# Performance work log

Measured on AMD Instinct MI355X. Metric: run time of the kernel, lower is better.

Reference implementation:

```python
import jax, jax.numpy as jnp
import numpy as np

DROPOUT_P = 0.1
SCALE = 0.0625  # 1/sqrt(256)


def setup_inputs() -> dict:
    key = jax.random.key(0)
    kq, kk, kv, km, ku = jax.random.split(key, 5)
    B, Sq, Sk, D, Dv = 64, 1024, 1024, 256, 256
    q = jax.random.normal(kq, (B, Sq, D), dtype=jnp.float32)
    k = jax.random.normal(kk, (B, Sk, D), dtype=jnp.float32)
    v = jax.random.normal(kv, (B, Sk, Dv), dtype=jnp.float32)
    mask = jax.random.randint(km, (B, Sk), 0, 2, dtype=jnp.int32)
    drop_u = jax.random.uniform(ku, (B, Sq, Sk), dtype=jnp.float32)
    return {"q": q, "k": k, "v": v, "mask": mask, "drop_u": drop_u}


def reference(q, k, v, mask, drop_u):
    # attn scores: [B, Sq, Sk]
    attn = jnp.einsum("bqd,bkd->bqk", q, k) * SCALE
    # additive padding mask broadcast over queries
    mmask = -1e9 * (1.0 - mask.astype(attn.dtype))  # [B, Sk]
    attn = attn + mmask[:, None, :]
    attn = jax.nn.softmax(attn, axis=-1)
    # inverted dropout with pre-sampled uniforms (deterministic)
    keep = (drop_u >= DROPOUT_P).astype(attn.dtype) / (1.0 - DROPOUT_P)
    attn = attn * keep
    out = jnp.einsum("bqk,bkv->bqv", attn, v)
    return out
```

## Files before the change

kernel.cpp:

```cpp
#include <hip/hip_runtime.h>
#include <hip/hip_bf16.h>
#include <stdint.h>

typedef __bf16 bf16_t;
typedef bf16_t bf16x8 __attribute__((ext_vector_type(8)));
typedef bf16_t bf16x4 __attribute__((ext_vector_type(4)));
typedef float floatx4 __attribute__((ext_vector_type(4)));

#define B_  64
#define SQ  1024
#define SK  1024
#define D_  256
#define DV  256
#define TK  32
#define NT  32
#define SCALE_F 0.0625f
#define NMASK   (-1.0e9f)
#define KEEP_F  (1.0f/0.9f)
#define THRESH  0.1f

#define AS1(p) ((const __attribute__((address_space(1))) uint32_t*)(p))
#define AS3(p) ((__attribute__((address_space(3))) uint32_t*)(p))

#define RAW_BARRIER() __asm__ volatile("s_barrier" ::: "memory")
#define WAIT_VM(N)    __asm__ volatile("s_waitcnt vmcnt(" #N ")" ::: "memory")
#define WAIT_LGKM0()  __asm__ volatile("s_waitcnt lgkmcnt(0)" ::: "memory")

__device__ __forceinline__ void gload16(const void* g, void* lds) {
    __builtin_amdgcn_global_load_lds(AS1(g), AS3(lds), 16, 0, 0);
}

template<int CTRL>
__device__ __forceinline__ float dpp_f(float x) {
    int y = __builtin_amdgcn_update_dpp(0, __float_as_int(x), CTRL, 0xF, 0xF, true);
    return __int_as_float(y);
}
__device__ __forceinline__ float rowsum16(float v) {
    v += dpp_f<0x128>(v);
    v += dpp_f<0x124>(v);
    v += dpp_f<0x4E>(v);
    v += dpp_f<0xB1>(v);
    return v;
}
__device__ __forceinline__ float rowmax16(float v) {
    v = fmaxf(v, dpp_f<0x128>(v));
    v = fmaxf(v, dpp_f<0x124>(v));
    v = fmaxf(v, dpp_f<0x4E>(v));
    v = fmaxf(v, dpp_f<0xB1>(v));
    return v;
}

__global__ __launch_bounds__(256) void prepass(
    const float* __restrict__ k, const float* __restrict__ v,
    bf16_t* __restrict__ ktiles, bf16_t* __restrict__ vtiles)
{
    __shared__ bf16_t Vls[32 * 258];
    const int bid = blockIdx.x;
    const int tid = threadIdx.x;
    if (bid < 2048) {
        const int r = tid >> 3;
        const float* src = k + ((size_t)(bid * 32 + r)) * D_ + (tid & 7) * 32;
        char* dst = (char*)ktiles + ((size_t)bid) * 16384;
        #pragma unroll
        for (int gl = 0; gl < 4; ++gl) {
            float4 a = *(const float4*)(src + gl * 8);
            float4 b4 = *(const float4*)(src + gl * 8 + 4);
            bf16x8 f;
            f[0]=(bf16_t)a.x;  f[1]=(bf16_t)a.y;  f[2]=(bf16_t)a.z;  f[3]=(bf16_t)a.w;
            f[4]=(bf16_t)b4.x; f[5]=(bf16_t)b4.y; f[6]=(bf16_t)b4.z; f[7]=(bf16_t)b4.w;
            int g = (tid & 7) * 4 + gl;
            *(bf16x8*)(dst + r * 512 + ((g ^ (r & 7)) * 16)) = f;
        }
    } else {
        const int bid2 = bid - 2048;
        const int kk = tid >> 3, dv0 = (tid & 7) * 32;
        const float* src = v + ((size_t)(bid2 * 32 + kk)) * DV + dv0;
        #pragma unroll
        for (int j = 0; j < 8; ++j) {
            float4 a = *(const float4*)(src + j * 4);
            bf16x4 f4;
            f4[0]=(bf16_t)a.x; f4[1]=(bf16_t)a.y; f4[2]=(bf16_t)a.z; f4[3]=(bf16_t)a.w;
            *(bf16x4*)(&Vls[kk * 258 + dv0 + j * 4]) = f4;
        }
        __syncthreads();
        char* dst = (char*)vtiles + ((size_t)bid2) * 16384;
        #pragma unroll
        for (int c = 0; c < 4; ++c) {
            int dv = c * 64 + (tid >> 2);
            int gphys = tid & 3;
            int glog = gphys ^ ((dv >> 1) & 3);
            bf16x8 f;
            #pragma unroll
            for (int jj = 0; jj < 8; ++jj) f[jj] = Vls[(glog * 8 + jj) * 258 + dv];
            *(bf16x8*)(dst + dv * 64 + gphys * 16) = f;
        }
    }
}

__global__ __launch_bounds__(256, 3) void attn_main(
    const float* __restrict__ q, const int* __restrict__ mask,
    const float* __restrict__ du, const bf16_t* __restrict__ ktiles,
    const bf16_t* __restrict__ vtiles, float* __restrict__ out)
{
    __shared__ char smem[53248];
    char* KsB = smem;
    char* VtB = smem + 16384;
    char* DuB = smem + 32768;
    char* PsB = smem + 49152;

    const int bid  = blockIdx.x;
    const int b    = bid >> 4;
    const int qt   = bid & 15;
    const int tid  = threadIdx.x;
    const int wave = tid >> 6;
    const int lane = tid & 63;
    const int col  = lane & 15;
    const int quad = lane >> 4;

    bf16x8 qf[8];
    {
        const float* qp = q + ((size_t)(b*SQ + qt*64 + wave*16 + col))*D_ + quad*8;
        #pragma unroll
        for (int c = 0; c < 8; ++c) {
            float4 a  = *(const float4*)(qp + c*32);
            float4 b4 = *(const float4*)(qp + c*32 + 4);
            bf16x8 f;
            f[0]=(bf16_t)(a.x*SCALE_F);  f[1]=(bf16_t)(a.y*SCALE_F);
            f[2]=(bf16_t)(a.z*SCALE_F);  f[3]=(bf16_t)(a.w*SCALE_F);
            f[4]=(bf16_t)(b4.x*SCALE_F); f[5]=(bf16_t)(b4.y*SCALE_F);
            f[6]=(bf16_t)(b4.z*SCALE_F); f[7]=(bf16_t)(b4.w*SCALE_F);
            qf[c] = f;
        }
    }

    floatx4 o_acc[16];
    #pragma unroll
    for (int i = 0; i < 16; ++i) o_acc[i] = (floatx4){0.f,0.f,0.f,0.f};
    float m_i[4] = {-1e30f,-1e30f,-1e30f,-1e30f};
    float l_i[4] = {0.f,0.f,0.f,0.f};

    const size_t tbase = (size_t)(b * NT) * 16384;

    #define ISSUE_K(t) do { \
        const char* g_ = (const char*)ktiles + tbase + (size_t)(t)*16384 + wave*4096 + lane*16; \
        char* l_ = KsB + wave*4096; \
        gload16(g_, l_); gload16(g_+1024, l_+1024); \
        gload16(g_+2048, l_+2048); gload16(g_+3072, l_+3072); } while(0)

    #define ISSUE_V(t) do { \
        const char* g_ = (const char*)vtiles + tbase + (size_t)(t)*16384 + wave*4096 + lane*16; \
        char* l_ = VtB + wave*4096; \
        gload16(g_, l_); gload16(g_+1024, l_+1024); \
        gload16(g_+2048, l_+2048); gload16(g_+3072, l_+3072); } while(0)

    #define ISSUE_DU(t, buf) do { \
        char* l_ = DuB + (buf)*8192 + wave*2048; \
        _Pragma("unroll") \
        for (int s_ = 0; s_ < 2; ++s_) { \
            int row_ = wave*16 + s_*8 + (lane>>3); \
            int cl_ = (lane & 7) ^ (row_ & 7); \
            const char* g_ = (const char*)du + \
                (((size_t)(b*SQ + qt*64 + row_))*SK + (t)*TK + cl_*4)*4; \
            gload16(g_, l_ + s_*1024); \
        } } while(0)

    ISSUE_K(0);
    ISSUE_DU(0, 0);
    int mcur0 = mask[b*SK + col];
    int mcur1 = mask[b*SK + 16 + col];
    ISSUE_V(0);

    for (int kt = 0; kt < NT; ++kt) {
        const int tn = (kt + 1 < NT) ? kt + 1 : NT - 1;

        WAIT_VM(4);
        RAW_BARRIER();

        ISSUE_DU(tn, (kt + 1) & 1);
        int mn0 = mask[b*SK + tn*TK + col];
        int mn1 = mask[b*SK + tn*TK + 16 + col];

        floatx4 s0 = (floatx4){0,0,0,0}, s1 = (floatx4){0,0,0,0};
        #pragma unroll
        for (int c = 0; c < 8; ++c) {
            const int g0 = c*4 + quad;
            const int r0 = col, r1 = col + 16;
            bf16x8 kf0 = *(const bf16x8*)(KsB + r0*512 + ((g0 ^ (r0 & 7)) * 16));
            bf16x8 kf1 = *(const bf16x8*)(KsB + r1*512 + ((g0 ^ (r1 & 7)) * 16));
            s0 = __builtin_amdgcn_mfma_f32_16x16x32_bf16(qf[c], kf0, s0, 0,0,0);
            s1 = __builtin_amdgcn_mfma_f32_16x16x32_bf16(qf[c], kf1, s1, 0,0,0);
        }

        const float mm0 = mcur0 ? 0.f : NMASK;
        const float mm1 = mcur1 ? 0.f : NMASK;
        const char* duB = DuB + (kt & 1) * 8192;
        float alpha[4];
        #pragma unroll
        for (int i = 0; i < 4; ++i) {
            float sv0 = s0[i] + mm0;
            float sv1 = s1[i] + mm1;
            float mx = rowmax16(fmaxf(sv0, sv1));
            float mnew = fmaxf(m_i[i], mx);
            alpha[i] = __expf(m_i[i] - mnew);
            m_i[i] = mnew;
            float p0 = __expf(sv0 - mnew);
            float p1 = __expf(sv1 - mnew);
            float rs = rowsum16(p0 + p1);
            l_i[i] = l_i[i] * alpha[i] + rs;

            const int row = wave*16 + quad*4 + i;
            const int k0 = col, k1 = col + 16;
            float u0 = *(const float*)(duB + row*128 + (((k0>>2) ^ (row & 7)) * 16) + (k0 & 3)*4);
            float u1 = *(const float*)(duB + row*128 + (((k1>>2) ^ (row & 7)) * 16) + (k1 & 3)*4);
            p0 *= (u0 >= THRESH) ? KEEP_F : 0.f;
            p1 *= (u1 >= THRESH) ? KEEP_F : 0.f;
            *(bf16_t*)(PsB + row*64 + (((k0>>3) ^ ((row>>1) & 3)) * 16) + (k0 & 7)*2) = (bf16_t)p0;
            *(bf16_t*)(PsB + row*64 + (((k1>>3) ^ ((row>>1) & 3)) * 16) + (k1 & 7)*2) = (bf16_t)p1;
        }
        {
            floatx4 av = {alpha[0], alpha[1], alpha[2], alpha[3]};
            #pragma unroll
            for (int blk = 0; blk < 16; ++blk) o_acc[blk] *= av;
        }

        WAIT_LGKM0();
        RAW_BARRIER();
        ISSUE_K(tn);

        WAIT_VM(8);
        RAW_BARRIER();

        {
            const int prow = wave*16 + col;
            bf16x8 pf = *(const bf16x8*)(PsB + prow*64 + ((quad ^ ((prow>>1) & 3)) * 16));
            #pragma unroll
            for (int blk = 0; blk < 16; ++blk) {
                const int dv = blk*16 + col;
                bf16x8 vf = *(const bf16x8*)(VtB + dv*64 + ((quad ^ ((dv>>1) & 3)) * 16));
                o_acc[blk] = __builtin_amdgcn_mfma_f32_16x16x32_bf16(pf, vf, o_acc[blk], 0,0,0);
            }
        }

        WAIT_LGKM0();
        RAW_BARRIER();
        ISSUE_V(tn);

        mcur0 = mn0; mcur1 = mn1;
    }
    WAIT_VM(0);

    float inv_l[4];
    #pragma unroll
    for (int i = 0; i < 4; ++i) inv_l[i] = 1.f / l_i[i];
    float* op = out + ((size_t)(b*SQ + qt*64 + wave*16 + quad*4))*DV + col;
    #pragma unroll
    for (int blk = 0; blk < 16; ++blk) {
        #pragma unroll
        for (int i = 0; i < 4; ++i)
            op[(size_t)i*DV + blk*16] = o_acc[blk][i] * inv_l[i];
    }
    #undef ISSUE_K
    #undef ISSUE_V
    #undef ISSUE_DU
}

extern "C" void kernel_launch(void* const* d_in, const int* in_sizes, int n_in,
                              void* d_out, int out_size, void* d_ws, size_t ws_size,
                              hipStream_t stream) {
    const float* q    = (const float*)d_in[0];
    const float* k    = (const float*)d_in[1];
    const float* v    = (const float*)d_in[2];
    const int*   mask = (const int*)d_in[3];
    const float* du   = (const float*)d_in[4];
    float* out = (float*)d_out;

    bf16_t* ktiles = (bf16_t*)d_ws;
    bf16_t* vtiles = (bf16_t*)((char*)d_ws + (size_t)33554432);

    hipLaunchKernelGGL(prepass, dim3(4096), dim3(256), 0, stream, k, v, ktiles, vtiles);
    hipLaunchKernelGGL(attn_main, dim3(B_ * (SQ/64)), dim3(256), 0, stream,
                       q, mask, du, ktiles, vtiles, out);
}
```

Measured before the change: 662.2 us.

## Pack dropout uniforms into bitmasks in prepass and defer softmax rescaling

A third prepass section turns the fp32 dropout uniforms into one bit per element. The main kernel then reads one 32-bit word per row per tile straight into registers, where it used to stage fp32 tiles in LDS. The output and row-sum rescale is now skipped unless some row max grows by more than a threshold (lazy rescaling). LDS use drops and occupancy is raised from 3 to 4 blocks per CU. The prepass still has to read the full uniform tensor once, so the gain depends on the main kernel's bottleneck and on the extra bitmask write and read.

```diff
diff --git a/kernel.cpp b/kernel.cpp
--- a/kernel.cpp
+++ b/kernel.cpp
@@ -6,6 +6,7 @@
 typedef bf16_t bf16x8 __attribute__((ext_vector_type(8)));
 typedef bf16_t bf16x4 __attribute__((ext_vector_type(4)));
 typedef float floatx4 __attribute__((ext_vector_type(4)));
+typedef uint32_t uint32x4 __attribute__((ext_vector_type(4)));
 
 #define B_  64
 #define SQ  1024
@@ -18,6 +19,7 @@
 #define NMASK   (-1.0e9f)
 #define KEEP_F  (1.0f/0.9f)
 #define THRESH  0.1f
+#define DEFER_THR 3.0f
 
 #define AS1(p) ((const __attribute__((address_space(1))) uint32_t*)(p))
 #define AS3(p) ((__attribute__((address_space(3))) uint32_t*)(p))
@@ -51,8 +53,8 @@
 }
 
 __global__ __launch_bounds__(256) void prepass(
-    const float* __restrict__ k, const float* __restrict__ v,
-    bf16_t* __restrict__ ktiles, bf16_t* __restrict__ vtiles)
+    const float* __restrict__ k, const float* __restrict__ v, const float* __restrict__ du,
+    bf16_t* __restrict__ ktiles, bf16_t* __restrict__ vtiles, uint32_t* __restrict__ dubits)
 {
     __shared__ bf16_t Vls[32 * 258];
     const int bid = blockIdx.x;
@@ -71,7 +73,7 @@
             int g = (tid & 7) * 4 + gl;
             *(bf16x8*)(dst + r * 512 + ((g ^ (r & 7)) * 16)) = f;
         }
-    } else {
+    } else if (bid < 4096) {
         const int bid2 = bid - 2048;
         const int kk = tid >> 3, dv0 = (tid & 7) * 32;
         const float* src = v + ((size_t)(bid2 * 32 + kk)) * DV + dv0;
@@ -94,19 +96,36 @@
             for (int jj = 0; jj < 8; ++jj) f[jj] = Vls[(glog * 8 + jj) * 258 + dv];
             *(bf16x8*)(dst + dv * 64 + gphys * 16) = f;
         }
+    } else {
+        const int w0 = (bid - 4096) * 1024 + tid * 4;
+        const float* src = du + (size_t)w0 * 32;
+        uint32x4 bits;
+        #pragma unroll
+        for (int j = 0; j < 4; ++j) {
+            uint32_t m = 0;
+            #pragma unroll
+            for (int e = 0; e < 32; e += 4) {
+                float4 f = *(const float4*)(src + j * 32 + e);
+                m |= (f.x >= THRESH ? 1u : 0u) << e;
+                m |= (f.y >= THRESH ? 1u : 0u) << (e + 1);
+                m |= (f.z >= THRESH ? 1u : 0u) << (e + 2);
+                m |= (f.w >= THRESH ? 1u : 0u) << (e + 3);
+            }
+            bits[j] = m;
+        }
+        *(uint32x4*)(dubits + w0) = bits;
     }
 }
 
-__global__ __launch_bounds__(256, 3) void attn_main(
+__global__ __launch_bounds__(256, 4) void attn_main(
     const float* __restrict__ q, const int* __restrict__ mask,
-    const float* __restrict__ du, const bf16_t* __restrict__ ktiles,
+    const uint32_t* __restrict__ dubits, const bf16_t* __restrict__ ktiles,
     const bf16_t* __restrict__ vtiles, float* __restrict__ out)
 {
-    __shared__ char smem[53248];
+    __shared__ char smem[36864];
     char* KsB = smem;
     char* VtB = smem + 16384;
-    char* DuB = smem + 32768;
-    char* PsB = smem + 49152;
+    char* PsB = smem + 32768;
 
     const int bid  = blockIdx.x;
     const int b    = bid >> 4;
@@ -140,6 +159,7 @@
     float l_i[4] = {0.f,0.f,0.f,0.f};
 
     const size_t tbase = (size_t)(b * NT) * 16384;
+    const uint32_t* dub = dubits + ((size_t)(b*SQ + qt*64 + wave*16 + quad*4)) * 32;
 
     #define ISSUE_K(t) do { \
         const char* g_ = (const char*)ktiles + tbase + (size_t)(t)*16384 + wave*4096 + lane*16; \
@@ -153,19 +173,10 @@
         gload16(g_, l_); gload16(g_+1024, l_+1024); \
         gload16(g_+2048, l_+2048); gload16(g_+3072, l_+3072); } while(0)
 
-    #define ISSUE_DU(t, buf) do { \
-        char* l_ = DuB + (buf)*8192 + wave*2048; \
-        _Pragma("unroll") \
-        for (int s_ = 0; s_ < 2; ++s_) { \
-            int row_ = wave*16 + s_*8 + (lane>>3); \
-            int cl_ = (lane & 7) ^ (row_ & 7); \
-            const char* g_ = (const char*)du + \
-                (((size_t)(b*SQ + qt*64 + row_))*SK + (t)*TK + cl_*4)*4; \
-            gload16(g_, l_ + s_*1024); \
-        } } while(0)
-
     ISSUE_K(0);
-    ISSUE_DU(0, 0);
+    uint32_t dwc[4];
+    #pragma unroll
+    for (int i = 0; i < 4; ++i) dwc[i] = dub[i*32 + 0];
     int mcur0 = mask[b*SK + col];
     int mcur1 = mask[b*SK + 16 + col];
     ISSUE_V(0);
@@ -176,7 +187,9 @@
         WAIT_VM(4);
         RAW_BARRIER();
 
-        ISSUE_DU(tn, (kt + 1) & 1);
+        uint32_t dwn[4];
+        #pragma unroll
+        for (int i = 0; i < 4; ++i) dwn[i] = dub[i*32 + tn];
         int mn0 = mask[b*SK + tn*TK + col];
         int mn1 = mask[b*SK + tn*TK + 16 + col];
 
@@ -193,41 +206,52 @@
 
         const float mm0 = mcur0 ? 0.f : NMASK;
         const float mm1 = mcur1 ? 0.f : NMASK;
-        const char* duB = DuB + (kt & 1) * 8192;
-        float alpha[4];
+        float sv0[4], sv1[4], mxr[4];
         #pragma unroll
         for (int i = 0; i < 4; ++i) {
-            float sv0 = s0[i] + mm0;
-            float sv1 = s1[i] + mm1;
-            float mx = rowmax16(fmaxf(sv0, sv1));
-            float mnew = fmaxf(m_i[i], mx);
-            alpha[i] = __expf(m_i[i] - mnew);
-            m_i[i] = mnew;
-            float p0 = __expf(sv0 - mnew);
-            float p1 = __expf(sv1 - mnew);
+            sv0[i] = s0[i] + mm0;
+            sv1[i] = s1[i] + mm1;
+            mxr[i] = rowmax16(fmaxf(sv0[i], sv1[i]));
+        }
+        float g = mxr[0] - m_i[0];
+        g = fmaxf(g, mxr[1] - m_i[1]);
+        g = fmaxf(g, mxr[2] - m_i[2]);
+        g = fmaxf(g, mxr[3] - m_i[3]);
+        if (__any(g > DEFER_THR)) {
+            float alpha[4];
+            #pragma unroll
+            for (int i = 0; i < 4; ++i) {
+                float mnew = fmaxf(m_i[i], mxr[i]);
+                alpha[i] = __expf(m_i[i] - mnew);
+                m_i[i] = mnew;
+                l_i[i] *= alpha[i];
+            }
+            floatx4 av = {alpha[0], alpha[1], alpha[2], alpha[3]};
+            #pragma unroll
+            for (int blk = 0; blk < 16; ++blk) o_acc[blk] *= av;
+        }
+        #pragma unroll
+        for (int i = 0; i < 4; ++i) {
+            float p0 = __expf(sv0[i] - m_i[i]);
+            float p1 = __expf(sv1[i] - m_i[i]);
             float rs = rowsum16(p0 + p1);
-            l_i[i] = l_i[i] * alpha[i] + rs;
+            l_i[i] += rs;
+
+            uint32_t wb = dwc[i];
+            p0 = ((wb >> col) & 1u)        ? p0 * KEEP_F : 0.f;
+            p1 = ((wb >> (col + 16)) & 1u) ? p1 * KEEP_F : 0.f;
 
             const int row = wave*16 + quad*4 + i;
             const int k0 = col, k1 = col + 16;
-            float u0 = *(const float*)(duB + row*128 + (((k0>>2) ^ (row & 7)) * 16) + (k0 & 3)*4);
-            float u1 = *(const float*)(duB + row*128 + (((k1>>2) ^ (row & 7)) * 16) + (k1 & 3)*4);
-            p0 *= (u0 >= THRESH) ? KEEP_F : 0.f;
-            p1 *= (u1 >= THRESH) ? KEEP_F : 0.f;
             *(bf16_t*)(PsB + row*64 + (((k0>>3) ^ ((row>>1) & 3)) * 16) + (k0 & 7)*2) = (bf16_t)p0;
             *(bf16_t*)(PsB + row*64 + (((k1>>3) ^ ((row>>1) & 3)) * 16) + (k1 & 7)*2) = (bf16_t)p1;
-        }
-        {
-            floatx4 av = {alpha[0], alpha[1], alpha[2], alpha[3]};
-            #pragma unroll
-            for (int blk = 0; blk < 16; ++blk) o_acc[blk] *= av;
         }
 
         WAIT_LGKM0();
         RAW_BARRIER();
         ISSUE_K(tn);
 
-        WAIT_VM(8);
+        WAIT_VM(10);
         RAW_BARRIER();
 
         {
@@ -245,6 +269,8 @@
         RAW_BARRIER();
         ISSUE_V(tn);
 
+        #pragma unroll
+        for (int i = 0; i < 4; ++i) dwc[i] = dwn[i];
         mcur0 = mn0; mcur1 = mn1;
     }
     WAIT_VM(0);
@@ -261,7 +287,6 @@
     }
     #undef ISSUE_K
     #undef ISSUE_V
-    #undef ISSUE_DU
 }
 
 extern "C" void kernel_launch(void* const* d_in, const int* in_sizes, int n_in,
@@ -274,10 +299,11 @@
     const float* du   = (const float*)d_in[4];
     float* out = (float*)d_out;
 
-    bf16_t* ktiles = (bf16_t*)d_ws;
-    bf16_t* vtiles = (bf16_t*)((char*)d_ws + (size_t)33554432);
-
-    hipLaunchKernelGGL(prepass, dim3(4096), dim3(256), 0, stream, k, v, ktiles, vtiles);
+    bf16_t*   ktiles = (bf16_t*)d_ws;
+    bf16_t*   vtiles = (bf16_t*)((char*)d_ws + (size_t)33554432);
+    uint32_t* dubits = (uint32_t*)((char*)d_ws + (size_t)67108864);
+
+    hipLaunchKernelGGL(prepass, dim3(6144), dim3(256), 0, stream, k, v, du, ktiles, vtiles, dubits);
     hipLaunchKernelGGL(attn_main, dim3(B_ * (SQ/64)), dim3(256), 0, stream,
-                       q, mask, du, ktiles, vtiles, out);
-}
+                       q, mask, dubits, ktiles, vtiles, out);
+}
```

Result: slower. 774.9 us (+17.0%).
